# Kernel tuning notes

Measured on AMD Instinct MI355X. Metric: run time of the kernel, lower is better.

The kernel has to match this reference:

```python
import jax, jax.numpy as jnp
import numpy as np

N_NODES = 20000
N_EDGES = 320000
C_Z = 256
C_EDGE = 64
HEADS = 8
C_OUT = 32  # HEADS * C_OUT == C_Z
LN_EPS = 1e-5


def setup_inputs() -> dict:
    key = jax.random.key(0)
    ks = jax.random.split(key, 16)
    d_feat = 2 * C_Z + C_EDGE  # 576
    hc = HEADS * C_OUT
    s = 0.02
    return {
        "x": jax.random.normal(ks[0], (N_NODES, C_Z), jnp.float32),
        "p": jax.random.normal(ks[1], (N_NODES, C_Z), jnp.float32),
        "edge_attr": jax.random.normal(ks[2], (N_EDGES, C_EDGE), jnp.float32),
        "edge_index": jax.random.randint(ks[3], (2, N_EDGES), 0, N_NODES, jnp.int32),
        "ln_w": jnp.ones((d_feat,), jnp.float32),
        "ln_b": jnp.zeros((d_feat,), jnp.float32),
        "Wq": jax.random.normal(ks[4], (C_Z, hc), jnp.float32) * s,
        "bq": jnp.zeros((hc,), jnp.float32),
        "Wk": jax.random.normal(ks[5], (d_feat, hc), jnp.float32) * s,
        "bk": jnp.zeros((hc,), jnp.float32),
        "Wv": jax.random.normal(ks[6], (d_feat, hc), jnp.float32) * s,
        "bv": jnp.zeros((hc,), jnp.float32),
        "We": jax.random.normal(ks[7], (C_EDGE, hc), jnp.float32) * s,
        "W1": jax.random.normal(ks[8], (C_Z, 2 * C_Z), jnp.float32) * s,
        "b1": jnp.zeros((2 * C_Z,), jnp.float32),
        "W2": jax.random.normal(ks[9], (2 * C_Z, C_Z), jnp.float32) * s,
        "b2": jnp.zeros((C_Z,), jnp.float32),
    }


def _layer_norm(v, w, b):
    mu = jnp.mean(v, axis=-1, keepdims=True)
    var = jnp.var(v, axis=-1, keepdims=True)
    return (v - mu) * jax.lax.rsqrt(var + LN_EPS) * w + b


def reference(x, p, edge_attr, edge_index, ln_w, ln_b, Wq, bq, Wk, bk, Wv, bv, We, W1, b1, W2, b2):
    src, dst = edge_index[0], edge_index[1]
    n = x.shape[0]
    # edge-gather + layernorm of concat features [E, 2*c_z + c_edge]
    feat = jnp.concatenate([edge_attr, x[src], p[dst]], axis=-1)
    feat = _layer_norm(feat, ln_w, ln_b)
    q = (x @ Wq + bq).reshape(-1, HEADS, C_OUT)        # [N,H,C]
    k = (feat @ Wk + bk).reshape(-1, HEADS, C_OUT)     # [E,H,C]
    v = (feat @ Wv + bv).reshape(-1, HEADS, C_OUT)     # [E,H,C]
    # per-edge scores and scatter-softmax over destination node (src index)
    scores = jnp.sum(q[src] * k, axis=-1) / np.sqrt(C_OUT)  # [E,H]
    smax = jax.ops.segment_max(scores, src, num_segments=n)  # [N,H]
    ex = jnp.exp(scores - smax[src])
    ssum = jax.ops.segment_sum(ex, src, num_segments=n)
    alpha = ex / ssum[src]                                   # [E,H]
    eg = (edge_attr @ We).reshape(-1, HEADS, C_OUT)          # [E,H,C]
    m = alpha[..., None] * (v * eg)                          # [E,H,C]
    out = jax.ops.segment_sum(m, src, num_segments=n).reshape(n, HEADS * C_OUT)
    # output MLP: Linear -> SiLU -> Linear
    h = jax.nn.silu(out @ W1 + b1)
    return h @ W2 + b2
```

## Files before the change

kernel.cpp:

```cpp
#include <hip/hip_runtime.h>

#define N_NODES 20000
#define N_EDGES 320000

typedef __attribute__((ext_vector_type(8))) short bf16x8;
typedef __attribute__((ext_vector_type(4))) float f32x4;

__device__ __forceinline__ float4 ld4(const float* p) { return *(const float4*)p; }

__device__ __forceinline__ unsigned short f2bf(float f) {
  unsigned int u = __float_as_uint(f);
  return (unsigned short)((u + 0x7FFFu + ((u >> 16) & 1u)) >> 16);
}
__device__ __forceinline__ float bf2f(unsigned short b) {
  return __uint_as_float(((unsigned int)b) << 16);
}
__device__ __forceinline__ float bflo(unsigned int u) { return __uint_as_float(u << 16); }
__device__ __forceinline__ float bfhi(unsigned int u) { return __uint_as_float(u & 0xFFFF0000u); }

template<bool SILU>
__global__ __launch_bounds__(256) void gemm64(
    const float* __restrict__ A, const float* __restrict__ W,
    const float* __restrict__ bias, float* __restrict__ C,
    int M, int K, int N)
{
  __shared__ __align__(16) float As[32][68];
  __shared__ __align__(16) float Ws[32][68];
  const int m0 = blockIdx.y * 64, n0 = blockIdx.x * 64;
  const int t = threadIdx.x;
  const int tx = t & 15, ty = t >> 4;
  float acc[4][4] = {{0.f,0.f,0.f,0.f},{0.f,0.f,0.f,0.f},{0.f,0.f,0.f,0.f},{0.f,0.f,0.f,0.f}};

  for (int k0 = 0; k0 < K; k0 += 32) {
    {
      const int r = t >> 3, c4 = (t & 7) * 4;
      #pragma unroll
      for (int rr = 0; rr < 64; rr += 32) {
        const int gm = m0 + r + rr;
        float4 v = make_float4(0.f, 0.f, 0.f, 0.f);
        if (gm < M) v = ld4(A + (size_t)gm * K + k0 + c4);
        As[c4 + 0][r + rr] = v.x; As[c4 + 1][r + rr] = v.y;
        As[c4 + 2][r + rr] = v.z; As[c4 + 3][r + rr] = v.w;
      }
      const int wr = t >> 4, wc4 = (t & 15) * 4;
      #pragma unroll
      for (int rr = 0; rr < 32; rr += 16) {
        float4 v = ld4(W + (size_t)(k0 + wr + rr) * N + n0 + wc4);
        *(float4*)&Ws[wr + rr][wc4] = v;
      }
    }
    __syncthreads();
    #pragma unroll
    for (int kk = 0; kk < 32; ++kk) {
      float4 av = *(const float4*)&As[kk][ty * 4];
      float4 bv = *(const float4*)&Ws[kk][tx * 4];
      const float a[4] = {av.x, av.y, av.z, av.w};
      const float b[4] = {bv.x, bv.y, bv.z, bv.w};
      #pragma unroll
      for (int i = 0; i < 4; ++i)
        #pragma unroll
        for (int j = 0; j < 4; ++j)
          acc[i][j] += a[i] * b[j];
    }
    __syncthreads();
  }

  const float4 bv = ld4(bias + n0 + tx * 4);
  const float bb[4] = {bv.x, bv.y, bv.z, bv.w};
  #pragma unroll
  for (int i = 0; i < 4; ++i) {
    const int gm = m0 + ty * 4 + i;
    if (gm < M) {
      float o[4];
      #pragma unroll
      for (int j = 0; j < 4; ++j) {
        float v = acc[i][j] + bb[j];
        if (SILU) v = v / (1.f + __expf(-v));
        o[j] = v;
      }
      float4 ov = make_float4(o[0], o[1], o[2], o[3]);
      *(float4*)&C[(size_t)gm * N + n0 + tx * 4] = ov;
    }
  }
}

__global__ __launch_bounds__(256) void prep_weights(
    const float* __restrict__ Wk, const float* __restrict__ Wv,
    const float* __restrict__ We,
    unsigned short* __restrict__ wkT, unsigned short* __restrict__ wvT,
    unsigned short* __restrict__ weT)
{
  const int id = blockIdx.x * 256 + threadIdx.x;
  if (id < 576 * 256) {
    const int k = id >> 8, c = id & 255;
    wkT[(size_t)c * 576 + k] = f2bf(Wk[id]);
    wvT[(size_t)c * 576 + k] = f2bf(Wv[id]);
  }
  if (id < 64 * 256) {
    const int k = id >> 8, c = id & 255;
    weT[(size_t)c * 64 + k] = f2bf(We[id]);
  }
}

__global__ __launch_bounds__(256) void edge_mfma_kernel(
    const float* __restrict__ x, const float* __restrict__ p,
    const float* __restrict__ ea, const int* __restrict__ eidx,
    const float* __restrict__ lnw, const float* __restrict__ lnb,
    const unsigned short* __restrict__ wkT, const float* __restrict__ bk,
    const unsigned short* __restrict__ wvT, const float* __restrict__ bv,
    const unsigned short* __restrict__ weT, const float* __restrict__ q,
    float* __restrict__ ssum, unsigned short* __restrict__ mbuf)
{
  __shared__ __align__(16) unsigned short featb[32][584];
  __shared__ __align__(16) float qs[32][260];
  __shared__ __align__(16) unsigned short eab[32][72];
  __shared__ int src_s[32], dst_s[32];

  const int t = threadIdx.x;
  const int eb = blockIdx.x * 32;
  if (t < 32) src_s[t] = eidx[eb + t];
  else if (t < 64) dst_s[t - 32] = eidx[N_EDGES + eb + (t - 32)];
  __syncthreads();

  {
    const int cid0 = t >> 4, l16 = t & 15;
    #pragma unroll
    for (int it = 0; it < 18; ++it) {
      const int cid = it * 16 + cid0;
      const int e = cid & 31;
      const int s = cid >> 5;
      const float* sp;
      if (s == 0)      sp = ea + (size_t)(eb + e) * 64 + l16 * 4;
      else if (s <= 4) sp = x + (size_t)src_s[e] * 256 + ((s - 1) * 16 + l16) * 4;
      else             sp = p + (size_t)dst_s[e] * 256 + ((s - 5) * 16 + l16) * 4;
      const float4 v = ld4(sp);
      uint2 pk;
      pk.x = (unsigned int)f2bf(v.x) | ((unsigned int)f2bf(v.y) << 16);
      pk.y = (unsigned int)f2bf(v.z) | ((unsigned int)f2bf(v.w) << 16);
      *(uint2*)&featb[e][(s * 16 + l16) * 4] = pk;
      if (s == 0) *(uint2*)&eab[e][l16 * 4] = pk;
    }
    #pragma unroll
    for (int it = 0; it < 8; ++it) {
      const int idx = it * 256 + t;
      const int e = idx >> 6, c4 = idx & 63;
      const float4 v = ld4(q + (size_t)src_s[e] * 256 + c4 * 4);
      *(float4*)&qs[e][c4 * 4] = v;
    }
  }
  __syncthreads();

  {
    const int e = t >> 3, g = t & 7;
    float sum = 0.f, sq = 0.f;
    #pragma unroll
    for (int i = 0; i < 9; ++i) {
      const uint4 u = *(const uint4*)&featb[e][(g + 8 * i) * 8];
      const float f0 = bflo(u.x), f1 = bfhi(u.x), f2 = bflo(u.y), f3 = bfhi(u.y);
      const float f4 = bflo(u.z), f5 = bfhi(u.z), f6 = bflo(u.w), f7 = bfhi(u.w);
      sum += (f0 + f1) + (f2 + f3) + (f4 + f5) + (f6 + f7);
      sq += f0*f0 + f1*f1 + f2*f2 + f3*f3 + f4*f4 + f5*f5 + f6*f6 + f7*f7;
    }
    sum += __shfl_xor(sum, 1); sq += __shfl_xor(sq, 1);
    sum += __shfl_xor(sum, 2); sq += __shfl_xor(sq, 2);
    sum += __shfl_xor(sum, 4); sq += __shfl_xor(sq, 4);
    const float mu = sum * (1.f / 576.f);
    const float var = sq * (1.f / 576.f) - mu * mu;
    const float rstd = rsqrtf(var + 1e-5f);
    #pragma unroll
    for (int i = 0; i < 9; ++i) {
      const int ch = g + 8 * i;
      uint4 u = *(const uint4*)&featb[e][ch * 8];
      const float4 w0 = ld4(lnw + ch * 8), w1 = ld4(lnw + ch * 8 + 4);
      const float4 b0 = ld4(lnb + ch * 8), b1 = ld4(lnb + ch * 8 + 4);
      const float o0 = (bflo(u.x) - mu) * rstd * w0.x + b0.x;
      const float o1 = (bfhi(u.x) - mu) * rstd * w0.y + b0.y;
      const float o2 = (bflo(u.y) - mu) * rstd * w0.z + b0.z;
      const float o3 = (bfhi(u.y) - mu) * rstd * w0.w + b0.w;
      const float o4 = (bflo(u.z) - mu) * rstd * w1.x + b1.x;
      const float o5 = (bfhi(u.z) - mu) * rstd * w1.y + b1.y;
      const float o6 = (bflo(u.w) - mu) * rstd * w1.z + b1.z;
      const float o7 = (bfhi(u.w) - mu) * rstd * w1.w + b1.w;
      u.x = (unsigned int)f2bf(o0) | ((unsigned int)f2bf(o1) << 16);
      u.y = (unsigned int)f2bf(o2) | ((unsigned int)f2bf(o3) << 16);
      u.z = (unsigned int)f2bf(o4) | ((unsigned int)f2bf(o5) << 16);
      u.w = (unsigned int)f2bf(o6) | ((unsigned int)f2bf(o7) << 16);
      *(uint4*)&featb[e][ch * 8] = u;
    }
  }
  __syncthreads();

  const int wid = t >> 6, l = t & 63;
  const int lr = l & 15, lg = l >> 4;
  const int j0 = wid * 64;

  f32x4 kacc[2][4];
  #pragma unroll
  for (int nt = 0; nt < 4; ++nt) {
    const float bb = bk[j0 + nt * 16 + lr];
    f32x4 c; c[0] = bb; c[1] = bb; c[2] = bb; c[3] = bb;
    kacc[0][nt] = c; kacc[1][nt] = c;
  }
  #pragma unroll 2
  for (int ks = 0; ks < 18; ++ks) {
    const bf16x8 a0 = *(const bf16x8*)&featb[lr][ks * 32 + lg * 8];
    const bf16x8 a1 = *(const bf16x8*)&featb[16 + lr][ks * 32 + lg * 8];
    #pragma unroll
    for (int nt = 0; nt < 4; ++nt) {
      const bf16x8 bf = *(const bf16x8*)(wkT + (size_t)(j0 + nt * 16 + lr) * 576 + ks * 32 + lg * 8);
      kacc[0][nt] = __builtin_amdgcn_mfma_f32_16x16x32_bf16(a0, bf, kacc[0][nt], 0, 0, 0);
      kacc[1][nt] = __builtin_amdgcn_mfma_f32_16x16x32_bf16(a1, bf, kacc[1][nt], 0, 0, 0);
    }
  }

  float exv[2][4][2];
  #pragma unroll
  for (int mt = 0; mt < 2; ++mt)
    #pragma unroll
    for (int r = 0; r < 4; ++r) {
      const int e = mt * 16 + lg * 4 + r;
      float s0 = kacc[mt][0][r] * qs[e][j0 + lr]      + kacc[mt][1][r] * qs[e][j0 + 16 + lr];
      float s1 = kacc[mt][2][r] * qs[e][j0 + 32 + lr] + kacc[mt][3][r] * qs[e][j0 + 48 + lr];
      s0 += __shfl_xor(s0, 1); s1 += __shfl_xor(s1, 1);
      s0 += __shfl_xor(s0, 2); s1 += __shfl_xor(s1, 2);
      s0 += __shfl_xor(s0, 4); s1 += __shfl_xor(s1, 4);
      s0 += __shfl_xor(s0, 8); s1 += __shfl_xor(s1, 8);
      exv[mt][r][0] = __expf(s0 * 0.17677669529663687f);
      exv[mt][r][1] = __expf(s1 * 0.17677669529663687f);
    }
  if (lr == 0) {
    #pragma unroll
    for (int mt = 0; mt < 2; ++mt)
      #pragma unroll
      for (int r = 0; r < 4; ++r) {
        const int sn = src_s[mt * 16 + lg * 4 + r];
        atomicAdd(&ssum[(size_t)sn * 8 + wid * 2 + 0], exv[mt][r][0]);
        atomicAdd(&ssum[(size_t)sn * 8 + wid * 2 + 1], exv[mt][r][1]);
      }
  }

  f32x4 vacc[2][4];
  #pragma unroll
  for (int nt = 0; nt < 4; ++nt) {
    const float bb = bv[j0 + nt * 16 + lr];
    f32x4 c; c[0] = bb; c[1] = bb; c[2] = bb; c[3] = bb;
    vacc[0][nt] = c; vacc[1][nt] = c;
  }
  #pragma unroll 2
  for (int ks = 0; ks < 18; ++ks) {
    const bf16x8 a0 = *(const bf16x8*)&featb[lr][ks * 32 + lg * 8];
    const bf16x8 a1 = *(const bf16x8*)&featb[16 + lr][ks * 32 + lg * 8];
    #pragma unroll
    for (int nt = 0; nt < 4; ++nt) {
      const bf16x8 bf = *(const bf16x8*)(wvT + (size_t)(j0 + nt * 16 + lr) * 576 + ks * 32 + lg * 8);
      vacc[0][nt] = __builtin_amdgcn_mfma_f32_16x16x32_bf16(a0, bf, vacc[0][nt], 0, 0, 0);
      vacc[1][nt] = __builtin_amdgcn_mfma_f32_16x16x32_bf16(a1, bf, vacc[1][nt], 0, 0, 0);
    }
  }

  f32x4 gacc[2][4];
  #pragma unroll
  for (int nt = 0; nt < 4; ++nt) {
    f32x4 c; c[0] = 0.f; c[1] = 0.f; c[2] = 0.f; c[3] = 0.f;
    gacc[0][nt] = c; gacc[1][nt] = c;
  }
  #pragma unroll
  for (int ks = 0; ks < 2; ++ks) {
    const bf16x8 a0 = *(const bf16x8*)&eab[lr][ks * 32 + lg * 8];
    const bf16x8 a1 = *(const bf16x8*)&eab[16 + lr][ks * 32 + lg * 8];
    #pragma unroll
    for (int nt = 0; nt < 4; ++nt) {
      const bf16x8 bf = *(const bf16x8*)(weT + (size_t)(j0 + nt * 16 + lr) * 64 + ks * 32 + lg * 8);
      gacc[0][nt] = __builtin_amdgcn_mfma_f32_16x16x32_bf16(a0, bf, gacc[0][nt], 0, 0, 0);
      gacc[1][nt] = __builtin_amdgcn_mfma_f32_16x16x32_bf16(a1, bf, gacc[1][nt], 0, 0, 0);
    }
  }

  #pragma unroll
  for (int mt = 0; mt < 2; ++mt)
    #pragma unroll
    for (int nt = 0; nt < 4; ++nt)
      #pragma unroll
      for (int r = 0; r < 4; ++r) {
        const int e = eb + mt * 16 + lg * 4 + r;
        const float m = exv[mt][r][nt >> 1] * vacc[mt][nt][r] * gacc[mt][nt][r];
        mbuf[(size_t)e * 256 + j0 + nt * 16 + lr] = f2bf(m);
      }
}

__global__ void hist_kernel(const int* __restrict__ eidx, int* __restrict__ deg)
{
  const int e = blockIdx.x * 256 + threadIdx.x;
  if (e < N_EDGES) atomicAdd(&deg[eidx[e]], 1);
}

__global__ __launch_bounds__(1024) void scan_kernel(
    const int* __restrict__ deg, int* __restrict__ off, int* __restrict__ cursor)
{
  __shared__ int part[1024];
  const int t = threadIdx.x;
  const int base = t * 20;
  int s = 0;
  #pragma unroll 4
  for (int j = 0; j < 20; ++j) {
    const int n = base + j;
    if (n < N_NODES) s += deg[n];
  }
  part[t] = s;
  __syncthreads();
  for (int st = 1; st < 1024; st <<= 1) {
    int v = (t >= st) ? part[t - st] : 0;
    __syncthreads();
    part[t] += v;
    __syncthreads();
  }
  int run = (t == 0) ? 0 : part[t - 1];
  for (int j = 0; j < 20; ++j) {
    const int n = base + j;
    if (n < N_NODES) {
      off[n] = run;
      cursor[n] = run;
      run += deg[n];
    }
  }
  if (t == 1023) off[N_NODES] = part[1023];
}

__global__ void scatter_kernel(const int* __restrict__ eidx,
                               int* __restrict__ cursor, int* __restrict__ order)
{
  const int e = blockIdx.x * 256 + threadIdx.x;
  if (e < N_EDGES) {
    const int s = eidx[e];
    const int pos = atomicAdd(&cursor[s], 1);
    order[pos] = e;
  }
}

__global__ __launch_bounds__(64) void gather_kernel(
    const unsigned short* __restrict__ mbuf, const int* __restrict__ off,
    const int* __restrict__ order, const float* __restrict__ ssum,
    float* __restrict__ attn)
{
  const int n = blockIdx.x;
  const int t = threadIdx.x;
  const int c0 = t * 4;
  const int o0 = off[n], o1 = off[n + 1];
  float a0 = 0.f, a1 = 0.f, a2 = 0.f, a3 = 0.f;
  for (int j = o0; j < o1; ++j) {
    const int e = order[j];
    const ushort4 raw = *(const ushort4*)&mbuf[(size_t)e * 256 + c0];
    a0 += bf2f(raw.x); a1 += bf2f(raw.y); a2 += bf2f(raw.z); a3 += bf2f(raw.w);
  }
  const int h = c0 >> 5;
  float inv = 0.f;
  if (o1 > o0) inv = 1.f / ssum[(size_t)n * 8 + h];
  float4 o = make_float4(a0 * inv, a1 * inv, a2 * inv, a3 * inv);
  *(float4*)&attn[(size_t)n * 256 + c0] = o;
}

extern "C" void kernel_launch(void* const* d_in, const int* in_sizes, int n_in,
                              void* d_out, int out_size, void* d_ws, size_t ws_size,
                              hipStream_t stream)
{
  const float* x   = (const float*)d_in[0];
  const float* p   = (const float*)d_in[1];
  const float* ea  = (const float*)d_in[2];
  const int*   ei  = (const int*)d_in[3];
  const float* lnw = (const float*)d_in[4];
  const float* lnb = (const float*)d_in[5];
  const float* Wq  = (const float*)d_in[6];
  const float* bq  = (const float*)d_in[7];
  const float* Wk  = (const float*)d_in[8];
  const float* bk  = (const float*)d_in[9];
  const float* Wv  = (const float*)d_in[10];
  const float* bv  = (const float*)d_in[11];
  const float* We  = (const float*)d_in[12];
  const float* W1  = (const float*)d_in[13];
  const float* b1  = (const float*)d_in[14];
  const float* W2  = (const float*)d_in[15];
  const float* b2  = (const float*)d_in[16];
  float* out = (float*)d_out;

  float* q    = (float*)d_ws;
  float* attn = q + (size_t)N_NODES * 256;
  float* hbuf = attn + (size_t)N_NODES * 256;
  float* ssum = hbuf + (size_t)N_NODES * 512;
  int* deg    = (int*)(ssum + (size_t)N_NODES * 8);
  int* off    = deg + N_NODES;
  int* cursor = off + (N_NODES + 1);
  int* order  = cursor + N_NODES;
  size_t ihead = (size_t)(order + N_EDGES - (int*)d_ws);
  ihead = (ihead + 3) & ~(size_t)3;
  unsigned short* mbuf = (unsigned short*)((int*)d_ws + ihead);
  unsigned short* wkT = mbuf + (size_t)N_EDGES * 256;
  unsigned short* wvT = wkT + (size_t)256 * 576;
  unsigned short* weT = wvT + (size_t)256 * 576;

  hipMemsetAsync(ssum, 0, (size_t)N_NODES * 8 * sizeof(float), stream);
  hipMemsetAsync(deg, 0, (size_t)N_NODES * sizeof(int), stream);

  dim3 blk(256);
  prep_weights<<<dim3(576), blk, 0, stream>>>(Wk, Wv, We, wkT, wvT, weT);
  gemm64<false><<<dim3(4, 313), blk, 0, stream>>>(x, Wq, bq, q, N_NODES, 256, 256);
  hist_kernel<<<dim3((N_EDGES + 255) / 256), blk, 0, stream>>>(ei, deg);
  scan_kernel<<<dim3(1), dim3(1024), 0, stream>>>(deg, off, cursor);
  scatter_kernel<<<dim3((N_EDGES + 255) / 256), blk, 0, stream>>>(ei, cursor, order);
  edge_mfma_kernel<<<dim3(N_EDGES / 32), blk, 0, stream>>>(
      x, p, ea, ei, lnw, lnb, wkT, bk, wvT, bv, weT, q, ssum, mbuf);
  gather_kernel<<<dim3(N_NODES), dim3(64), 0, stream>>>(mbuf, off, order, ssum, attn);
  gemm64<true><<<dim3(8, 313), blk, 0, stream>>>(attn, W1, b1, hbuf, N_NODES, 256, 512);
  gemm64<false><<<dim3(4, 313), blk, 0, stream>>>(hbuf, W2, b2, out, N_NODES, 512, 256);
}
```

Measured before the change: 1.292 ms.

## Fuse K and V MFMA loops and load q directly into registers

Merges the separate K and V projection loops into one pass, so each LDS read of the feature A-fragments feeds both K and V MFMAs. The q shared-memory staging buffer is removed; each lane loads the q values it needs straight from global memory into registers at kernel start, which also frees about 33KB of LDS per block. The cost is more live accumulator registers, which may lower occupancy, plus scattered small global loads for q.

```diff
diff --git a/kernel.cpp b/kernel.cpp
--- a/kernel.cpp
+++ b/kernel.cpp
@@ -112,7 +112,6 @@
     float* __restrict__ ssum, unsigned short* __restrict__ mbuf)
 {
   __shared__ __align__(16) unsigned short featb[32][584];
-  __shared__ __align__(16) float qs[32][260];
   __shared__ __align__(16) unsigned short eab[32][72];
   __shared__ int src_s[32], dst_s[32];
 
@@ -121,6 +120,25 @@
   if (t < 32) src_s[t] = eidx[eb + t];
   else if (t < 64) dst_s[t - 32] = eidx[N_EDGES + eb + (t - 32)];
   __syncthreads();
+
+  const int wid = t >> 6, l = t & 63;
+  const int lr = l & 15, lg = l >> 4;
+  const int j0 = wid * 64;
+
+  int sn_r[2][4];
+  float qv[2][4][4];
+  #pragma unroll
+  for (int mt = 0; mt < 2; ++mt)
+    #pragma unroll
+    for (int r = 0; r < 4; ++r) {
+      const int sn = src_s[mt * 16 + lg * 4 + r];
+      sn_r[mt][r] = sn;
+      const float* qr = q + (size_t)sn * 256 + j0 + lr;
+      qv[mt][r][0] = qr[0];
+      qv[mt][r][1] = qr[16];
+      qv[mt][r][2] = qr[32];
+      qv[mt][r][3] = qr[48];
+    }
 
   {
     const int cid0 = t >> 4, l16 = t & 15;
@@ -139,13 +157,6 @@
       pk.y = (unsigned int)f2bf(v.z) | ((unsigned int)f2bf(v.w) << 16);
       *(uint2*)&featb[e][(s * 16 + l16) * 4] = pk;
       if (s == 0) *(uint2*)&eab[e][l16 * 4] = pk;
-    }
-    #pragma unroll
-    for (int it = 0; it < 8; ++it) {
-      const int idx = it * 256 + t;
-      const int e = idx >> 6, c4 = idx & 63;
-      const float4 v = ld4(q + (size_t)src_s[e] * 256 + c4 * 4);
-      *(float4*)&qs[e][c4 * 4] = v;
     }
   }
   __syncthreads();
@@ -190,26 +201,32 @@
   }
   __syncthreads();
 
-  const int wid = t >> 6, l = t & 63;
-  const int lr = l & 15, lg = l >> 4;
-  const int j0 = wid * 64;
-
-  f32x4 kacc[2][4];
+  f32x4 kacc[2][4], vacc[2][4];
   #pragma unroll
   for (int nt = 0; nt < 4; ++nt) {
-    const float bb = bk[j0 + nt * 16 + lr];
-    f32x4 c; c[0] = bb; c[1] = bb; c[2] = bb; c[3] = bb;
-    kacc[0][nt] = c; kacc[1][nt] = c;
-  }
-  #pragma unroll 2
-  for (int ks = 0; ks < 18; ++ks) {
-    const bf16x8 a0 = *(const bf16x8*)&featb[lr][ks * 32 + lg * 8];
-    const bf16x8 a1 = *(const bf16x8*)&featb[16 + lr][ks * 32 + lg * 8];
-    #pragma unroll
-    for (int nt = 0; nt < 4; ++nt) {
-      const bf16x8 bf = *(const bf16x8*)(wkT + (size_t)(j0 + nt * 16 + lr) * 576 + ks * 32 + lg * 8);
-      kacc[0][nt] = __builtin_amdgcn_mfma_f32_16x16x32_bf16(a0, bf, kacc[0][nt], 0, 0, 0);
-      kacc[1][nt] = __builtin_amdgcn_mfma_f32_16x16x32_bf16(a1, bf, kacc[1][nt], 0, 0, 0);
+    const float bbk = bk[j0 + nt * 16 + lr];
+    const float bbv = bv[j0 + nt * 16 + lr];
+    f32x4 ck; ck[0] = bbk; ck[1] = bbk; ck[2] = bbk; ck[3] = bbk;
+    f32x4 cv; cv[0] = bbv; cv[1] = bbv; cv[2] = bbv; cv[3] = bbv;
+    kacc[0][nt] = ck; kacc[1][nt] = ck;
+    vacc[0][nt] = cv; vacc[1][nt] = cv;
+  }
+  {
+    const size_t wbase = (size_t)(j0 + lr) * 576 + lg * 8;
+    #pragma unroll 3
+    for (int ks = 0; ks < 18; ++ks) {
+      const bf16x8 a0 = *(const bf16x8*)&featb[lr][ks * 32 + lg * 8];
+      const bf16x8 a1 = *(const bf16x8*)&featb[16 + lr][ks * 32 + lg * 8];
+      #pragma unroll
+      for (int nt = 0; nt < 4; ++nt) {
+        const size_t wo = wbase + (size_t)nt * 16 * 576 + ks * 32;
+        const bf16x8 bkf = *(const bf16x8*)(wkT + wo);
+        const bf16x8 bvf = *(const bf16x8*)(wvT + wo);
+        kacc[0][nt] = __builtin_amdgcn_mfma_f32_16x16x32_bf16(a0, bkf, kacc[0][nt], 0, 0, 0);
+        kacc[1][nt] = __builtin_amdgcn_mfma_f32_16x16x32_bf16(a1, bkf, kacc[1][nt], 0, 0, 0);
+        vacc[0][nt] = __builtin_amdgcn_mfma_f32_16x16x32_bf16(a0, bvf, vacc[0][nt], 0, 0, 0);
+        vacc[1][nt] = __builtin_amdgcn_mfma_f32_16x16x32_bf16(a1, bvf, vacc[1][nt], 0, 0, 0);
+      }
     }
   }
 
@@ -218,9 +235,8 @@
   for (int mt = 0; mt < 2; ++mt)
     #pragma unroll
     for (int r = 0; r < 4; ++r) {
-      const int e = mt * 16 + lg * 4 + r;
-      float s0 = kacc[mt][0][r] * qs[e][j0 + lr]      + kacc[mt][1][r] * qs[e][j0 + 16 + lr];
-      float s1 = kacc[mt][2][r] * qs[e][j0 + 32 + lr] + kacc[mt][3][r] * qs[e][j0 + 48 + lr];
+      float s0 = kacc[mt][0][r] * qv[mt][r][0] + kacc[mt][1][r] * qv[mt][r][1];
+      float s1 = kacc[mt][2][r] * qv[mt][r][2] + kacc[mt][3][r] * qv[mt][r][3];
       s0 += __shfl_xor(s0, 1); s1 += __shfl_xor(s1, 1);
       s0 += __shfl_xor(s0, 2); s1 += __shfl_xor(s1, 2);
       s0 += __shfl_xor(s0, 4); s1 += __shfl_xor(s1, 4);
@@ -233,29 +249,10 @@
     for (int mt = 0; mt < 2; ++mt)
       #pragma unroll
       for (int r = 0; r < 4; ++r) {
-        const int sn = src_s[mt * 16 + lg * 4 + r];
+        const int sn = sn_r[mt][r];
         atomicAdd(&ssum[(size_t)sn * 8 + wid * 2 + 0], exv[mt][r][0]);
         atomicAdd(&ssum[(size_t)sn * 8 + wid * 2 + 1], exv[mt][r][1]);
       }
-  }
-
-  f32x4 vacc[2][4];
-  #pragma unroll
-  for (int nt = 0; nt < 4; ++nt) {
-    const float bb = bv[j0 + nt * 16 + lr];
-    f32x4 c; c[0] = bb; c[1] = bb; c[2] = bb; c[3] = bb;
-    vacc[0][nt] = c; vacc[1][nt] = c;
-  }
-  #pragma unroll 2
-  for (int ks = 0; ks < 18; ++ks) {
-    const bf16x8 a0 = *(const bf16x8*)&featb[lr][ks * 32 + lg * 8];
-    const bf16x8 a1 = *(const bf16x8*)&featb[16 + lr][ks * 32 + lg * 8];
-    #pragma unroll
-    for (int nt = 0; nt < 4; ++nt) {
-      const bf16x8 bf = *(const bf16x8*)(wvT + (size_t)(j0 + nt * 16 + lr) * 576 + ks * 32 + lg * 8);
-      vacc[0][nt] = __builtin_amdgcn_mfma_f32_16x16x32_bf16(a0, bf, vacc[0][nt], 0, 0, 0);
-      vacc[1][nt] = __builtin_amdgcn_mfma_f32_16x16x32_bf16(a1, bf, vacc[1][nt], 0, 0, 0);
-    }
   }
 
   f32x4 gacc[2][4];
```

Result: slower. 1.514 ms (+17.2%).
